# Optimization experiments

Hardware: AMD Instinct MI355X
Metric: run time of the kernel (lower is better)

## Reference

```python
import jax, jax.numpy as jnp
import numpy as np

COND_SIZE = 512
LR_SCALE = 1.0 / np.sqrt(COND_SIZE)  # equalized-lr scale for the style linear
EPS = 1e-8


def _style(condition, w):
    # lr_equal(nn.Linear(cond_size, in_size, bias=False)): runtime weight scale 1/sqrt(fan_in)
    return (condition @ w.T) * LR_SCALE  # [B, Cin]


def _mod_demod_conv(x, w, b, style):
    # x [B,Cin,H,W], w [Cout,Cin,3,3], style [B,Cin]
    wmod = w[None] * style[:, None, :, None, None]               # [B,Cout,Cin,3,3]
    demod = jax.lax.rsqrt(jnp.sum(wmod * wmod, axis=(2, 3, 4)) + EPS)  # [B,Cout]
    wmod = wmod * demod[:, :, None, None, None]
    conv1 = lambda xi, wi: jax.lax.conv_general_dilated(
        xi[None], wi, window_strides=(1, 1), padding='SAME')[0]
    out = jax.vmap(conv1)(x, wmod)                                # per-sample weights
    return out + b[None, :, None, None]


def setup_inputs() -> dict:
    key = jax.random.key(0)
    ks = jax.random.split(key, 12)
    B, Cin, Cout, H, W = 8, 128, 64, 256, 256
    return {
        'inputs': jax.random.normal(ks[0], (B, Cin, H, W), jnp.float32),
        'condition': jax.random.normal(ks[1], (B, COND_SIZE), jnp.float32),
        'cond_w0': jax.random.normal(ks[2], (Cin, COND_SIZE), jnp.float32),
        'cond_w1': jax.random.normal(ks[3], (Cin, COND_SIZE), jnp.float32),
        'conv_w0': jax.random.normal(ks[4], (Cin, Cin, 3, 3), jnp.float32) * 0.05,
        'conv_b0': jnp.zeros((Cin,), jnp.float32),
        'conv_w1': jax.random.normal(ks[5], (Cout, Cin, 3, 3), jnp.float32) * 0.05,
        'conv_b1': jnp.zeros((Cout,), jnp.float32),
        'noise_scale0': jax.random.normal(ks[6], (Cin,), jnp.float32),
        'noise_scale1': jax.random.normal(ks[7], (Cout,), jnp.float32),
        'noise0': jax.random.normal(ks[8], (B, Cin, H, W), jnp.float32),
        'noise1': jax.random.normal(ks[9], (B, Cout, H, W), jnp.float32),
        'rgb_w': jax.random.normal(ks[10], (3, Cout), jnp.float32) * 0.05,
        'rgb_b': jnp.zeros((3,), jnp.float32),
    }


def reference(inputs, condition, cond_w0, cond_w1, conv_w0, conv_b0,
              conv_w1, conv_b1, noise_scale0, noise_scale1,
              noise0, noise1, rgb_w, rgb_b):
    # block 0: modulated/demodulated 3x3 conv + channel-scaled noise injection
    out = _mod_demod_conv(inputs, conv_w0, conv_b0, _style(condition, cond_w0))
    out = out + noise0 * noise_scale0[None, :, None, None]
    # block 1
    out = _mod_demod_conv(out, conv_w1, conv_b1, _style(condition, cond_w1))
    out = out + noise1 * noise_scale1[None, :, None, None]
    # 1x1 to-RGB conv
    rgb = jnp.einsum('bchw,oc->bohw', out, rgb_w) + rgb_b[None, :, None, None]
    return (out, rgb)
```

## Files before the change

kernel.cpp:

```cpp
#include <hip/hip_runtime.h>
#include <stdint.h>
#include <stddef.h>


typedef __bf16 bf16;
typedef __bf16 bf16x8 __attribute__((ext_vector_type(8)));
typedef float  f32x4  __attribute__((ext_vector_type(4)));

#define AS1 __attribute__((address_space(1)))
#define AS3 __attribute__((address_space(3)))

#define OFF_A1    0ull
#define OFF_WT0   134217728ull
#define OFF_WT1   134512640ull
#define OFF_S0    134660096ull
#define OFF_S1    134664192ull
#define OFF_DM0   134668288ull
#define OFF_DM1   134672384ull
#define OFF_WSQ0  134674432ull
#define OFF_WSQ1  134739968ull
#define OFF_ZP    134772736ull

static __device__ __forceinline__ void gload_lds16(const void* src, void* ldsdst) {
  __builtin_amdgcn_global_load_lds((const AS1 void*)src, (AS3 void*)ldsdst, 16, 0, 0);
}

__global__ __launch_bounds__(256) void k_prep1(
    const float* __restrict__ cond, const float* __restrict__ cw0,
    const float* __restrict__ cw1, const float* __restrict__ w0,
    const float* __restrict__ w1, float* __restrict__ s0, float* __restrict__ s1,
    bf16* __restrict__ wt0, bf16* __restrict__ wt1,
    float* __restrict__ wsq0, float* __restrict__ wsq1, float* __restrict__ zp)
{
  int idx = blockIdx.x * 256 + threadIdx.x;
  if (idx < 2048) {
    int which = idx >> 10; int b = (idx >> 7) & 7; int c = idx & 127;
    const float* cw = which ? cw1 : cw0;
    const float* cp = cond + b * 512;
    const float* wp = cw + c * 512;
    float acc = 0.f;
    for (int j = 0; j < 512; ++j) acc += cp[j] * wp[j];
    (which ? s1 : s0)[b * 128 + c] = acc * 0.044194173824159216f;
    return;
  }
  idx -= 2048;
  if (idx < 147456) {
    int t = idx >> 14;
    wt0[idx] = (bf16)w0[(idx & 16383) * 9 + t];
    return;
  }
  idx -= 147456;
  if (idx < 73728) {
    int t = idx >> 13;
    wt1[idx] = (bf16)w1[(idx & 8191) * 9 + t];
    return;
  }
  idx -= 73728;
  if (idx < 16384) {
    const float* p = w0 + idx * 9; float a = 0.f;
    #pragma unroll
    for (int t = 0; t < 9; ++t) a += p[t] * p[t];
    wsq0[idx] = a; return;
  }
  idx -= 16384;
  if (idx < 8192) {
    const float* p = w1 + idx * 9; float a = 0.f;
    #pragma unroll
    for (int t = 0; t < 9; ++t) a += p[t] * p[t];
    wsq1[idx] = a; return;
  }
  idx -= 8192;
  if (idx < 64) zp[idx] = 0.f;
}

__global__ __launch_bounds__(256) void k_prep2(
    const float* __restrict__ s0, const float* __restrict__ s1,
    const float* __restrict__ wsq0, const float* __restrict__ wsq1,
    float* __restrict__ dm0, float* __restrict__ dm1)
{
  int idx = blockIdx.x * 256 + threadIdx.x;
  if (idx < 1024) {
    int b = idx >> 7, co = idx & 127;
    const float* sp = s0 + b * 128; const float* wp = wsq0 + co * 128;
    float a = 0.f;
    for (int ci = 0; ci < 128; ++ci) { float s = sp[ci]; a += s * s * wp[ci]; }
    dm0[idx] = rsqrtf(a + 1e-8f);
  } else if (idx < 1536) {
    int j = idx - 1024; int b = j >> 6, co = j & 63;
    const float* sp = s1 + b * 128; const float* wp = wsq1 + co * 128;
    float a = 0.f;
    for (int ci = 0; ci < 128; ++ci) { float s = sp[ci]; a += s * s * wp[ci]; }
    dm1[j] = rsqrtf(a + 1e-8f);
  }
}

__global__ __launch_bounds__(256) void k_mod(
    const float* __restrict__ x, const float* __restrict__ s0, bf16* __restrict__ A0)
{
  __shared__ alignas(16) char lds[8192];
  int bid = blockIdx.x;
  int b = bid >> 11; int rem = bid & 2047; int h = rem >> 3; int wp0 = (rem & 7) << 5;
  int t = threadIdx.x;
  #pragma unroll
  for (int iter = 0; iter < 2; ++iter) {
    int idx = iter * 256 + t; int w = idx & 31; int chunk = idx >> 5;
    const float* xp = x + (((size_t)(b * 128 + chunk * 8)) << 16) + (h << 8) + wp0 + w;
    const float* sp = s0 + b * 128 + chunk * 8;
    bf16x8 v;
    #pragma unroll
    for (int i = 0; i < 8; ++i) v[i] = (bf16)(xp[(size_t)i << 16] * sp[i]);
    *(bf16x8*)(lds + w * 256 + ((chunk ^ (w & 7)) << 4)) = v;
  }
  __syncthreads();
  #pragma unroll
  for (int iter = 0; iter < 2; ++iter) {
    int idx = iter * 256 + t; int w = idx >> 4; int c = idx & 15;
    bf16x8 v = *(const bf16x8*)(lds + w * 256 + ((c ^ (w & 7)) << 4));
    *(bf16x8*)(A0 + ((((size_t)(b << 16)) + (h << 8) + wp0 + w) << 7) + (c << 3)) = v;
  }
}

constexpr int cDY[9] = {0,0,0,1,1,1,2,2,2};
constexpr int cDX[9] = {0,1,2,0,1,2,0,1,2};

static __device__ __forceinline__ void stage_tileA(
    const bf16* __restrict__ src, const bf16* __restrict__ zp, char* Abase,
    int b, int h0, int w0p, int wave, int lane)
{
  #pragma unroll
  for (int i = 0; i < 12; ++i) {
    int g = wave + (i << 2);
    if (g < 45) {
      int pin = (g << 2) + (lane >> 4); int j = lane & 15;
      int r = pin / 18; int c = pin - r * 18;
      int gh = h0 - 1 + r, gw = w0p - 1 + c;
      const bf16* s;
      if (((unsigned)gh < 256u) & ((unsigned)gw < 256u))
        s = src + ((((size_t)(b << 16)) + (gh << 8) + gw) << 7) + ((j ^ (pin & 7)) << 3);
      else
        s = zp;
      gload_lds16(s, Abase + (size_t)g * 1024);
    }
  }
}

__global__ __launch_bounds__(256, 2) void k_conv0(
    const bf16* __restrict__ A0, const bf16* __restrict__ wt,
    const float* __restrict__ dm, const float* __restrict__ bias,
    const float* __restrict__ noise, const float* __restrict__ nsc,
    const float* __restrict__ s1, const bf16* __restrict__ zp,
    bf16* __restrict__ A1)
{
  __shared__ alignas(16) char lds[62464];
  char* Abase = lds;
  char* Bb0 = lds + 46080;
  char* Bb1 = lds + 54272;

  int bid = blockIdx.x;
  int wg = (bid & 7) * 512 + (bid >> 3);
  int b = wg >> 9; int rem = wg & 511;
  int h0 = (rem >> 4) << 3; int w0p = (rem & 15) << 4;
  int tid = threadIdx.x; int wave = tid >> 6; int lane = tid & 63;

  stage_tileA(A0, zp, Abase, b, h0, w0p, wave, lane);
  {
    #pragma unroll
    for (int i = 0; i < 2; ++i) {
      int co_base = (wave << 4) + (i << 6);
      int co = co_base + (lane >> 2);
      int kgs = (lane & 3) ^ ((co >> 1) & 3);
      gload_lds16(wt + co * 128 + (kgs << 3), Bb0 + co_base * 64);
    }
  }
  __syncthreads();

  int m16 = lane & 15, kg = lane >> 4;
  int pb = (wave >> 1) << 6, cb = (wave & 1) << 6;
  int basePin[4];
  #pragma unroll
  for (int mr = 0; mr < 4; ++mr)
    basePin[mr] = ((pb >> 4) + mr) * 18 + m16;

  f32x4 acc[4][4] = {};
  #pragma unroll
  for (int s = 0; s < 36; ++s) {
    char* Bcur = (s & 1) ? Bb1 : Bb0;
    char* Bnxt = (s & 1) ? Bb0 : Bb1;
    if (s + 1 < 36) {
      const int t1 = (s + 1) >> 2, ci1 = ((s + 1) & 3) << 5;
      #pragma unroll
      for (int i = 0; i < 2; ++i) {
        int co_base = (wave << 4) + (i << 6);
        int co = co_base + (lane >> 2);
        int kgs = (lane & 3) ^ ((co >> 1) & 3);
        gload_lds16(wt + (t1 << 14) + co * 128 + ci1 + (kgs << 3),
                    Bnxt + co_base * 64);
      }
    }
    const int t = s >> 2, c4 = s & 3;
    const int dy = cDY[t], dx = cDX[t];
    bf16x8 a[4], bwv[4];
    #pragma unroll
    for (int mr = 0; mr < 4; ++mr) {
      int pin = basePin[mr] + dy * 18 + dx;
      int cc = (c4 << 2) + kg;
      a[mr] = *(const bf16x8*)(Abase + pin * 256 + ((cc ^ (pin & 7)) << 4));
    }
    #pragma unroll
    for (int nr = 0; nr < 4; ++nr) {
      int co = cb + nr * 16 + m16;
      int slot = kg ^ ((co >> 1) & 3);
      bwv[nr] = *(const bf16x8*)(Bcur + co * 64 + (slot << 4));
    }
    __builtin_amdgcn_s_setprio(1);
    #pragma unroll
    for (int mr = 0; mr < 4; ++mr)
      #pragma unroll
      for (int nr = 0; nr < 4; ++nr)
        acc[mr][nr] = __builtin_amdgcn_mfma_f32_16x16x32_bf16(
            a[mr], bwv[nr], acc[mr][nr], 0, 0, 0);
    __builtin_amdgcn_s_setprio(0);
    __syncthreads();
  }

  float* zl = (float*)lds;
  #pragma unroll
  for (int half = 0; half < 2; ++half) {
    if ((wave >> 1) == half) {
      #pragma unroll
      for (int nr = 0; nr < 4; ++nr) {
        int co = cb + nr * 16 + m16;
        float d = dm[(b << 7) + co], bb = bias[co];
        #pragma unroll
        for (int mr = 0; mr < 4; ++mr) {
          int p0 = mr * 16 + (kg << 2);
          #pragma unroll
          for (int r = 0; r < 4; ++r)
            zl[(p0 + r) * 129 + co] = acc[mr][nr][r] * d + bb;
        }
      }
    }
    __syncthreads();
    #pragma unroll 4
    for (int it = 0; it < 32; ++it) {
      int idx = it * 256 + tid; int co = idx >> 6; int p6 = idx & 63;
      int gh = h0 + (half << 2) + (p6 >> 4), gw = w0p + (p6 & 15);
      float n = noise[(((size_t)((b << 7) + co)) << 16) + (gh << 8) + gw];
      float y = zl[p6 * 129 + co] + n * nsc[co];
      zl[p6 * 129 + co] = y * s1[(b << 7) + co];
    }
    __syncthreads();
    #pragma unroll
    for (int it = 0; it < 4; ++it) {
      int idx = it * 256 + tid; int p6 = idx >> 4; int ch = idx & 15;
      int gh = h0 + (half << 2) + (p6 >> 4), gw = w0p + (p6 & 15);
      const float* zpt = zl + p6 * 129 + (ch << 3);
      bf16x8 v;
      #pragma unroll
      for (int i = 0; i < 8; ++i) v[i] = (bf16)zpt[i];
      *(bf16x8*)(A1 + ((((size_t)(b << 16)) + (gh << 8) + gw) << 7) + (ch << 3)) = v;
    }
    __syncthreads();
  }
}

__global__ __launch_bounds__(256, 2) void k_conv1(
    const bf16* __restrict__ A1, const bf16* __restrict__ wt,
    const float* __restrict__ dm, const float* __restrict__ bias,
    const float* __restrict__ noise, const float* __restrict__ nsc,
    const float* __restrict__ rgbw, const float* __restrict__ rgbb,
    const bf16* __restrict__ zp, float* __restrict__ out, float* __restrict__ rgb)
{
  __shared__ alignas(16) char lds[54272];
  char* Abase = lds;
  char* Bb0 = lds + 46080;
  char* Bb1 = lds + 50176;

  int bid = blockIdx.x;
  int wg = (bid & 7) * 512 + (bid >> 3);
  int b = wg >> 9; int rem = wg & 511;
  int h0 = (rem >> 4) << 3; int w0p = (rem & 15) << 4;
  int tid = threadIdx.x; int wave = tid >> 6; int lane = tid & 63;

  stage_tileA(A1, zp, Abase, b, h0, w0p, wave, lane);
  {
    int co_base = wave << 4;
    int co = co_base + (lane >> 2);
    int kgs = (lane & 3) ^ ((co >> 1) & 3);
    gload_lds16(wt + co * 128 + (kgs << 3), Bb0 + co_base * 64);
  }
  __syncthreads();

  int m16 = lane & 15, kg = lane >> 4;
  int pb = (wave >> 1) << 6, cb = (wave & 1) << 5;
  int basePin[4];
  #pragma unroll
  for (int mr = 0; mr < 4; ++mr)
    basePin[mr] = ((pb >> 4) + mr) * 18 + m16;

  f32x4 acc[4][2] = {};
  #pragma unroll
  for (int s = 0; s < 36; ++s) {
    char* Bcur = (s & 1) ? Bb1 : Bb0;
    char* Bnxt = (s & 1) ? Bb0 : Bb1;
    if (s + 1 < 36) {
      const int t1 = (s + 1) >> 2, ci1 = ((s + 1) & 3) << 5;
      int co_base = wave << 4;
      int co = co_base + (lane >> 2);
      int kgs = (lane & 3) ^ ((co >> 1) & 3);
      gload_lds16(wt + (t1 << 13) + co * 128 + ci1 + (kgs << 3),
                  Bnxt + co_base * 64);
    }
    const int t = s >> 2, c4 = s & 3;
    const int dy = cDY[t], dx = cDX[t];
    bf16x8 a[4], bwv[2];
    #pragma unroll
    for (int mr = 0; mr < 4; ++mr) {
      int pin = basePin[mr] + dy * 18 + dx;
      int cc = (c4 << 2) + kg;
      a[mr] = *(const bf16x8*)(Abase + pin * 256 + ((cc ^ (pin & 7)) << 4));
    }
    #pragma unroll
    for (int nr = 0; nr < 2; ++nr) {
      int co = cb + nr * 16 + m16;
      int slot = kg ^ ((co >> 1) & 3);
      bwv[nr] = *(const bf16x8*)(Bcur + co * 64 + (slot << 4));
    }
    __builtin_amdgcn_s_setprio(1);
    #pragma unroll
    for (int mr = 0; mr < 4; ++mr)
      #pragma unroll
      for (int nr = 0; nr < 2; ++nr)
        acc[mr][nr] = __builtin_amdgcn_mfma_f32_16x16x32_bf16(
            a[mr], bwv[nr], acc[mr][nr], 0, 0, 0);
    __builtin_amdgcn_s_setprio(0);
    __syncthreads();
  }

  float* zl = (float*)lds;
  #pragma unroll
  for (int nr = 0; nr < 2; ++nr) {
    int co = cb + nr * 16 + m16;
    float d = dm[(b << 6) + co], bb = bias[co];
    #pragma unroll
    for (int mr = 0; mr < 4; ++mr) {
      int p0 = pb + mr * 16 + (kg << 2);
      #pragma unroll
      for (int r = 0; r < 4; ++r)
        zl[(p0 + r) * 65 + co] = acc[mr][nr][r] * d + bb;
    }
  }
  __syncthreads();
  #pragma unroll 4
  for (int it = 0; it < 32; ++it) {
    int idx = it * 256 + tid; int co = idx >> 7; int p = idx & 127;
    int gh = h0 + (p >> 4), gw = w0p + (p & 15);
    size_t go = (((size_t)((b << 6) + co)) << 16) + (gh << 8) + gw;
    float y = zl[p * 65 + co] + noise[go] * nsc[co];
    zl[p * 65 + co] = y;
    out[go] = y;
  }
  __syncthreads();
  if (tid < 128) {
    int p = tid; int gh = h0 + (p >> 4), gw = w0p + (p & 15);
    float r0 = rgbb[0], r1 = rgbb[1], r2 = rgbb[2];
    for (int co = 0; co < 64; ++co) {
      float v = zl[p * 65 + co];
      r0 += v * rgbw[co]; r1 += v * rgbw[64 + co]; r2 += v * rgbw[128 + co];
    }
    size_t base = (((size_t)(b * 3)) << 16) + (gh << 8) + gw;
    rgb[base] = r0; rgb[base + (1 << 16)] = r1; rgb[base + (2 << 16)] = r2;
  }
}

extern "C" void kernel_launch(void* const* d_in, const int* in_sizes, int n_in,
                              void* d_out, int out_size, void* d_ws, size_t ws_size,
                              hipStream_t stream)
{
  const float* x      = (const float*)d_in[0];
  const float* cond   = (const float*)d_in[1];
  const float* cw0    = (const float*)d_in[2];
  const float* cw1    = (const float*)d_in[3];
  const float* w0     = (const float*)d_in[4];
  const float* b0     = (const float*)d_in[5];
  const float* w1     = (const float*)d_in[6];
  const float* b1     = (const float*)d_in[7];
  const float* ns0    = (const float*)d_in[8];
  const float* ns1    = (const float*)d_in[9];
  const float* noise0 = (const float*)d_in[10];
  const float* noise1 = (const float*)d_in[11];
  const float* rgbw   = (const float*)d_in[12];
  const float* rgbb   = (const float*)d_in[13];

  char* ws = (char*)d_ws;
  bf16*  A1   = (bf16*)(ws + OFF_A1);
  bf16*  WT0  = (bf16*)(ws + OFF_WT0);
  bf16*  WT1  = (bf16*)(ws + OFF_WT1);
  float* S0   = (float*)(ws + OFF_S0);
  float* S1   = (float*)(ws + OFF_S1);
  float* DM0  = (float*)(ws + OFF_DM0);
  float* DM1  = (float*)(ws + OFF_DM1);
  float* WSQ0 = (float*)(ws + OFF_WSQ0);
  float* WSQ1 = (float*)(ws + OFF_WSQ1);
  float* ZP   = (float*)(ws + OFF_ZP);

  float* out = (float*)d_out;
  float* rgb = out + 33554432;

  bf16* A0 = (bf16*)d_out;

  k_prep1<<<dim3(969), dim3(256), 0, stream>>>(cond, cw0, cw1, w0, w1,
                                               S0, S1, WT0, WT1, WSQ0, WSQ1, ZP);
  k_prep2<<<dim3(6), dim3(256), 0, stream>>>(S0, S1, WSQ0, WSQ1, DM0, DM1);
  k_mod<<<dim3(16384), dim3(256), 0, stream>>>(x, S0, A0);
  k_conv0<<<dim3(4096), dim3(256), 0, stream>>>(A0, WT0, DM0, b0, noise0, ns0,
                                                S1, (const bf16*)ZP, A1);
  k_conv1<<<dim3(4096), dim3(256), 0, stream>>>(A1, WT1, DM1, b1, noise1, ns1,
                                                rgbw, rgbb, (const bf16*)ZP, out, rgb);
}
```

Measured before the change: 492.7 us.

## Triple-buffer weight tiles in conv kernels with prefetch distance two

Measured after the change: 478.4 us. 2.9% less time.

```diff
diff --git a/kernel.cpp b/kernel.cpp
--- a/kernel.cpp
+++ b/kernel.cpp
@@ -151,10 +151,11 @@
     const float* __restrict__ s1, const bf16* __restrict__ zp,
     bf16* __restrict__ A1)
 {
-  __shared__ alignas(16) char lds[62464];
+  extern __shared__ __align__(16) char lds[];
   char* Abase = lds;
-  char* Bb0 = lds + 46080;
-  char* Bb1 = lds + 54272;
+  char* Bp0 = lds + 46080;
+  char* Bp1 = lds + 54272;
+  char* Bp2 = lds + 62464;
 
   int bid = blockIdx.x;
   int wg = (bid & 7) * 512 + (bid >> 3);
@@ -162,17 +163,23 @@
   int h0 = (rem >> 4) << 3; int w0p = (rem & 15) << 4;
   int tid = threadIdx.x; int wave = tid >> 6; int lane = tid & 63;
 
-  stage_tileA(A0, zp, Abase, b, h0, w0p, wave, lane);
-  {
+  auto stageB = [&](int s, char* dst) {
+    const int t = s >> 2, ci = (s & 3) << 5;
     #pragma unroll
     for (int i = 0; i < 2; ++i) {
       int co_base = (wave << 4) + (i << 6);
       int co = co_base + (lane >> 2);
       int kgs = (lane & 3) ^ ((co >> 1) & 3);
-      gload_lds16(wt + co * 128 + (kgs << 3), Bb0 + co_base * 64);
-    }
-  }
-  __syncthreads();
+      gload_lds16(wt + ((size_t)t << 14) + co * 128 + ci + (kgs << 3),
+                  dst + co_base * 64);
+    }
+  };
+
+  stage_tileA(A0, zp, Abase, b, h0, w0p, wave, lane);
+  stageB(0, Bp0);
+  stageB(1, Bp1);
+  asm volatile("s_waitcnt vmcnt(2)" ::: "memory");
+  __builtin_amdgcn_s_barrier();
 
   int m16 = lane & 15, kg = lane >> 4;
   int pb = (wave >> 1) << 6, cb = (wave & 1) << 6;
@@ -184,19 +191,7 @@
   f32x4 acc[4][4] = {};
   #pragma unroll
   for (int s = 0; s < 36; ++s) {
-    char* Bcur = (s & 1) ? Bb1 : Bb0;
-    char* Bnxt = (s & 1) ? Bb0 : Bb1;
-    if (s + 1 < 36) {
-      const int t1 = (s + 1) >> 2, ci1 = ((s + 1) & 3) << 5;
-      #pragma unroll
-      for (int i = 0; i < 2; ++i) {
-        int co_base = (wave << 4) + (i << 6);
-        int co = co_base + (lane >> 2);
-        int kgs = (lane & 3) ^ ((co >> 1) & 3);
-        gload_lds16(wt + (t1 << 14) + co * 128 + ci1 + (kgs << 3),
-                    Bnxt + co_base * 64);
-      }
-    }
+    char* Bcur = (s % 3 == 0) ? Bp0 : ((s % 3 == 1) ? Bp1 : Bp2);
     const int t = s >> 2, c4 = s & 3;
     const int dy = cDY[t], dx = cDX[t];
     bf16x8 a[4], bwv[4];
@@ -211,6 +206,11 @@
       int co = cb + nr * 16 + m16;
       int slot = kg ^ ((co >> 1) & 3);
       bwv[nr] = *(const bf16x8*)(Bcur + co * 64 + (slot << 4));
+    }
+    if (s + 2 < 36) {
+      const int sn = s + 2;
+      char* Bnxt = (sn % 3 == 0) ? Bp0 : ((sn % 3 == 1) ? Bp1 : Bp2);
+      stageB(sn, Bnxt);
     }
     __builtin_amdgcn_s_setprio(1);
     #pragma unroll
@@ -220,8 +220,15 @@
         acc[mr][nr] = __builtin_amdgcn_mfma_f32_16x16x32_bf16(
             a[mr], bwv[nr], acc[mr][nr], 0, 0, 0);
     __builtin_amdgcn_s_setprio(0);
-    __syncthreads();
-  }
+    if (s <= 33) {
+      asm volatile("s_waitcnt vmcnt(2)" ::: "memory");
+      __builtin_amdgcn_s_barrier();
+    } else if (s == 34) {
+      asm volatile("s_waitcnt vmcnt(0)" ::: "memory");
+      __builtin_amdgcn_s_barrier();
+    }
+  }
+  __syncthreads();
 
   float* zl = (float*)lds;
   #pragma unroll
@@ -271,10 +278,11 @@
     const float* __restrict__ rgbw, const float* __restrict__ rgbb,
     const bf16* __restrict__ zp, float* __restrict__ out, float* __restrict__ rgb)
 {
-  __shared__ alignas(16) char lds[54272];
+  __shared__ alignas(16) char lds[58368];
   char* Abase = lds;
-  char* Bb0 = lds + 46080;
-  char* Bb1 = lds + 50176;
+  char* Bp0 = lds + 46080;
+  char* Bp1 = lds + 50176;
+  char* Bp2 = lds + 54272;
 
   int bid = blockIdx.x;
   int wg = (bid & 7) * 512 + (bid >> 3);
@@ -282,14 +290,20 @@
   int h0 = (rem >> 4) << 3; int w0p = (rem & 15) << 4;
   int tid = threadIdx.x; int wave = tid >> 6; int lane = tid & 63;
 
-  stage_tileA(A1, zp, Abase, b, h0, w0p, wave, lane);
-  {
+  auto stageB = [&](int s, char* dst) {
+    const int t = s >> 2, ci = (s & 3) << 5;
     int co_base = wave << 4;
     int co = co_base + (lane >> 2);
     int kgs = (lane & 3) ^ ((co >> 1) & 3);
-    gload_lds16(wt + co * 128 + (kgs << 3), Bb0 + co_base * 64);
-  }
-  __syncthreads();
+    gload_lds16(wt + ((size_t)t << 13) + co * 128 + ci + (kgs << 3),
+                dst + co_base * 64);
+  };
+
+  stage_tileA(A1, zp, Abase, b, h0, w0p, wave, lane);
+  stageB(0, Bp0);
+  stageB(1, Bp1);
+  asm volatile("s_waitcnt vmcnt(1)" ::: "memory");
+  __builtin_amdgcn_s_barrier();
 
   int m16 = lane & 15, kg = lane >> 4;
   int pb = (wave >> 1) << 6, cb = (wave & 1) << 5;
@@ -301,16 +315,7 @@
   f32x4 acc[4][2] = {};
   #pragma unroll
   for (int s = 0; s < 36; ++s) {
-    char* Bcur = (s & 1) ? Bb1 : Bb0;
-    char* Bnxt = (s & 1) ? Bb0 : Bb1;
-    if (s + 1 < 36) {
-      const int t1 = (s + 1) >> 2, ci1 = ((s + 1) & 3) << 5;
-      int co_base = wave << 4;
-      int co = co_base + (lane >> 2);
-      int kgs = (lane & 3) ^ ((co >> 1) & 3);
-      gload_lds16(wt + (t1 << 13) + co * 128 + ci1 + (kgs << 3),
-                  Bnxt + co_base * 64);
-    }
+    char* Bcur = (s % 3 == 0) ? Bp0 : ((s % 3 == 1) ? Bp1 : Bp2);
     const int t = s >> 2, c4 = s & 3;
     const int dy = cDY[t], dx = cDX[t];
     bf16x8 a[4], bwv[2];
@@ -325,6 +330,11 @@
       int co = cb + nr * 16 + m16;
       int slot = kg ^ ((co >> 1) & 3);
       bwv[nr] = *(const bf16x8*)(Bcur + co * 64 + (slot << 4));
+    }
+    if (s + 2 < 36) {
+      const int sn = s + 2;
+      char* Bnxt = (sn % 3 == 0) ? Bp0 : ((sn % 3 == 1) ? Bp1 : Bp2);
+      stageB(sn, Bnxt);
     }
     __builtin_amdgcn_s_setprio(1);
     #pragma unroll
@@ -334,8 +344,15 @@
         acc[mr][nr] = __builtin_amdgcn_mfma_f32_16x16x32_bf16(
             a[mr], bwv[nr], acc[mr][nr], 0, 0, 0);
     __builtin_amdgcn_s_setprio(0);
-    __syncthreads();
-  }
+    if (s <= 33) {
+      asm volatile("s_waitcnt vmcnt(1)" ::: "memory");
+      __builtin_amdgcn_s_barrier();
+    } else if (s == 34) {
+      asm volatile("s_waitcnt vmcnt(0)" ::: "memory");
+      __builtin_amdgcn_s_barrier();
+    }
+  }
+  __syncthreads();
 
   float* zl = (float*)lds;
   #pragma unroll
@@ -409,12 +426,15 @@
 
   bf16* A0 = (bf16*)d_out;
 
+  hipFuncSetAttribute((const void*)k_conv0,
+                      hipFuncAttributeMaxDynamicSharedMemorySize, 70656);
+
   k_prep1<<<dim3(969), dim3(256), 0, stream>>>(cond, cw0, cw1, w0, w1,
                                                S0, S1, WT0, WT1, WSQ0, WSQ1, ZP);
   k_prep2<<<dim3(6), dim3(256), 0, stream>>>(S0, S1, WSQ0, WSQ1, DM0, DM1);
   k_mod<<<dim3(16384), dim3(256), 0, stream>>>(x, S0, A0);
-  k_conv0<<<dim3(4096), dim3(256), 0, stream>>>(A0, WT0, DM0, b0, noise0, ns0,
-                                                S1, (const bf16*)ZP, A1);
+  k_conv0<<<dim3(4096), dim3(256), 70656, stream>>>(A0, WT0, DM0, b0, noise0, ns0,
+                                                    S1, (const bf16*)ZP, A1);
   k_conv1<<<dim3(4096), dim3(256), 0, stream>>>(A1, WT1, DM1, b1, noise1, ns1,
                                                 rgbw, rgbb, (const bf16*)ZP, out, rgb);
 }
```
